# Kernel tuning notes

Measured on AMD Instinct MI355X. Metric: run time of the kernel, lower is better.

Reference implementation:

```python
import jax, jax.numpy as jnp
import numpy as np

B, T, D = 64, 512, 384
MAX_LEN = 4096


def setup_inputs() -> dict:
    key = jax.random.key(0)
    kx, kd = jax.random.split(key)
    x = jax.random.normal(kx, (B, T, D), dtype=jnp.float32)
    duration = jax.random.randint(kd, (B, T), 0, 8, dtype=jnp.int32)
    return {"x": x, "duration": duration, "max_len": MAX_LEN}


def reference(x, duration, max_len):
    # x: [B, T, D], duration: [B, T] int, max_len: python int
    # Cumsum trick replaces the per-row repeat_interleave + cat + pad:
    # token t of row b occupies output rows [csum[t-1], csum[t]).
    csum = jnp.cumsum(duration, axis=1)                       # [B, T]
    mel_len = csum[:, -1]                                     # [B]
    pos = jnp.arange(max_len, dtype=csum.dtype)               # [M]
    # For each output position m, index of source token: first t with csum[t] > m
    idx = jax.vmap(lambda c: jnp.searchsorted(c, pos, side="right"))(csum)  # [B, M]
    idx = jnp.minimum(idx, x.shape[1] - 1)
    out = jnp.take_along_axis(x, idx[:, :, None], axis=1)     # [B, M, D]
    mask = (pos[None, :] < mel_len[:, None])[:, :, None]      # [B, M, 1]
    out = jnp.where(mask, out, jnp.zeros((), dtype=out.dtype))
    return out, mel_len
```

## Files before the change

### kernel.cpp

```cpp
#include <hip/hip_runtime.h>


#define T_DIM 512
#define D_DIM 384
#define D4    (D_DIM / 4)
#define ROWS  64
#define BLOCK 512
#define ITER  ((ROWS * D4) / BLOCK)
#define NWAVE (BLOCK / 64)

typedef float vfloat4 __attribute__((ext_vector_type(4)));

__global__ __launch_bounds__(BLOCK) void lr_fused_kernel(
    const float* __restrict__ x,
    const int*   __restrict__ duration,
    float*       __restrict__ out,
    int B, int ML)
{
    __shared__ int s_wsum[NWAVE];
    __shared__ int s_idx[ROWS];

    const int b     = blockIdx.x % B;
    const int chunk = blockIdx.x / B;
    const int row0  = chunk * ROWS;
    const int tid   = threadIdx.x;
    const int lane  = tid & 63;
    const int wid   = tid >> 6;

    const int d = duration[b * T_DIM + tid];
    int v = d;
    #pragma unroll
    for (int off = 1; off < 64; off <<= 1) {
        int u = __shfl_up(v, off);
        if (lane >= off) v += u;
    }
    if (lane == 63) s_wsum[wid] = v;
    if (tid < ROWS) s_idx[tid] = -1;
    __syncthreads();

    int wprefix = 0, mel = 0;
    #pragma unroll
    for (int w = 0; w < NWAVE; ++w) {
        const int s = s_wsum[w];
        if (w < wid) wprefix += s;
        mel += s;
    }
    const int end   = wprefix + v;
    const int start = end - d;

    const int lo = start > row0        ? start : row0;
    const int hi = end < row0 + ROWS   ? end   : row0 + ROWS;
    for (int p = lo; p < hi; ++p) s_idx[p - row0] = tid;
    __syncthreads();

    if (chunk == 0 && tid == 0)
        out[(long long)B * ML * D_DIM + b] = (float)mel;

    const vfloat4* __restrict__ x4   = (const vfloat4*)x;
    vfloat4*       __restrict__ out4 = (vfloat4*)out;
    const long long out_base = ((long long)b * ML + row0) * D4;
    const long long x_base   = (long long)b * T_DIM * D4;

    #pragma unroll
    for (int i = 0; i < ITER; ++i) {
        const int flat = tid + i * BLOCK;
        const int r = flat / D4;
        const int j = flat - r * D4;
        const int t = s_idx[r];
        vfloat4 vv = (vfloat4)(0.f, 0.f, 0.f, 0.f);
        if (t >= 0) vv = x4[x_base + (long long)t * D4 + j];
        out4[out_base + flat] = vv;
    }
}

extern "C" void kernel_launch(void* const* d_in, const int* in_sizes, int n_in,
                              void* d_out, int out_size, void* d_ws, size_t ws_size,
                              hipStream_t stream) {
    const float* x   = (const float*)d_in[0];
    const int*   dur = (const int*)d_in[1];
    float*       out = (float*)d_out;
    (void)d_ws; (void)ws_size;

    const int B  = in_sizes[1] / T_DIM;
    const int ML = (out_size - B) / (B * D_DIM);

    const int grid = B * (ML / ROWS);
    hipLaunchKernelGGL(lr_fused_kernel, dim3(grid), dim3(BLOCK), 0, stream,
                       x, dur, out, B, ML);
}
```

Before: 419.5 us.

## Give each wave its own rows and compute the duration scan per wave

Each wave now loads all 512 durations as two int4 vectors per lane, does a serial 8-element prefix plus a wave-level scan, and builds an index table only for its own 16 output rows. This removes both block-wide __syncthreads and the cross-wave partial-sum exchange, so waves proceed independently. Blocks now cover 128 rows instead of 64, which halves the grid. The trade-off is that every wave repeats the full scan and issues redundant duration loads.

```diff
diff --git a/kernel.cpp b/kernel.cpp
--- a/kernel.cpp
+++ b/kernel.cpp
@@ -4,12 +4,14 @@
 #define T_DIM 512
 #define D_DIM 384
 #define D4    (D_DIM / 4)
-#define ROWS  64
+#define WR    16
 #define BLOCK 512
-#define ITER  ((ROWS * D4) / BLOCK)
 #define NWAVE (BLOCK / 64)
+#define ROWS_BLK (WR * NWAVE)
+#define ITER  ((WR * D4) / 64)
 
 typedef float vfloat4 __attribute__((ext_vector_type(4)));
+typedef int   vint4   __attribute__((ext_vector_type(4)));
 
 __global__ __launch_bounds__(BLOCK) void lr_fused_kernel(
     const float* __restrict__ x,
@@ -17,56 +19,59 @@
     float*       __restrict__ out,
     int B, int ML)
 {
-    __shared__ int s_wsum[NWAVE];
-    __shared__ int s_idx[ROWS];
+    __shared__ int s_idx[NWAVE][WR];
 
     const int b     = blockIdx.x % B;
     const int chunk = blockIdx.x / B;
-    const int row0  = chunk * ROWS;
     const int tid   = threadIdx.x;
     const int lane  = tid & 63;
     const int wid   = tid >> 6;
+    const int w0    = chunk * ROWS_BLK + wid * WR;
 
-    const int d = duration[b * T_DIM + tid];
-    int v = d;
+    const vint4* __restrict__ dur4 = (const vint4*)(duration + b * T_DIM);
+    const vint4 da = dur4[2 * lane];
+    const vint4 db = dur4[2 * lane + 1];
+    int d[8]   = {da.x, da.y, da.z, da.w, db.x, db.y, db.z, db.w};
+    int lcs[8];
+    lcs[0] = d[0];
+    #pragma unroll
+    for (int k = 1; k < 8; ++k) lcs[k] = lcs[k - 1] + d[k];
+    int incl = lcs[7];
     #pragma unroll
     for (int off = 1; off < 64; off <<= 1) {
-        int u = __shfl_up(v, off);
-        if (lane >= off) v += u;
+        const int u = __shfl_up(incl, off);
+        if (lane >= off) incl += u;
     }
-    if (lane == 63) s_wsum[wid] = v;
-    if (tid < ROWS) s_idx[tid] = -1;
-    __syncthreads();
+    const int E   = incl - lcs[7];
+    const int mel = __shfl(incl, 63);
 
-    int wprefix = 0, mel = 0;
+    if (lane < WR) s_idx[wid][lane] = -1;
+
     #pragma unroll
-    for (int w = 0; w < NWAVE; ++w) {
-        const int s = s_wsum[w];
-        if (w < wid) wprefix += s;
-        mel += s;
+    for (int k = 0; k < 8; ++k) {
+        const int e = E + lcs[k];
+        const int s = e - d[k];
+        const int lo = s > w0 ? s : w0;
+        const int hi = e < w0 + WR ? e : w0 + WR;
+        for (int p = lo; p < hi; ++p) s_idx[wid][p - w0] = 8 * lane + k;
     }
-    const int end   = wprefix + v;
-    const int start = end - d;
+    __builtin_amdgcn_wave_barrier();
+    __asm__ volatile("s_waitcnt lgkmcnt(0)" ::: "memory");
 
-    const int lo = start > row0        ? start : row0;
-    const int hi = end < row0 + ROWS   ? end   : row0 + ROWS;
-    for (int p = lo; p < hi; ++p) s_idx[p - row0] = tid;
-    __syncthreads();
-
-    if (chunk == 0 && tid == 0)
+    if (blockIdx.x < B && tid == 0)
         out[(long long)B * ML * D_DIM + b] = (float)mel;
 
     const vfloat4* __restrict__ x4   = (const vfloat4*)x;
     vfloat4*       __restrict__ out4 = (vfloat4*)out;
-    const long long out_base = ((long long)b * ML + row0) * D4;
+    const long long out_base = ((long long)b * ML + w0) * D4;
     const long long x_base   = (long long)b * T_DIM * D4;
 
-    #pragma unroll
+    #pragma unroll 12
     for (int i = 0; i < ITER; ++i) {
-        const int flat = tid + i * BLOCK;
+        const int flat = lane + i * 64;
         const int r = flat / D4;
         const int j = flat - r * D4;
-        const int t = s_idx[r];
+        const int t = s_idx[wid][r];
         vfloat4 vv = (vfloat4)(0.f, 0.f, 0.f, 0.f);
         if (t >= 0) vv = x4[x_base + (long long)t * D4 + j];
         out4[out_base + flat] = vv;
@@ -84,7 +89,7 @@
     const int B  = in_sizes[1] / T_DIM;
     const int ML = (out_size - B) / (B * D_DIM);
 
-    const int grid = B * (ML / ROWS);
+    const int grid = B * (ML / ROWS_BLK);
     hipLaunchKernelGGL(lr_fused_kernel, dim3(grid), dim3(BLOCK), 0, stream,
                        x, dur, out, B, ML);
 }
```

Result: slower. 443.6 us (+5.7%).
